# Performance work log

Hardware: AMD Instinct MI355X
Metric: run time of the kernel (lower is better)

## Reference

```python
import jax, jax.numpy as jnp
import numpy as np

LMAX = 6
BLOCK_SIZES = [(2 * l + 1) ** 2 for l in range(LMAX + 1)]  # [1,9,25,49,81,121,169], sum=455
IRREPS_DIM = sum(BLOCK_SIZES)


def setup_inputs() -> dict:
    key = jax.random.key(0)
    k1, k2, k3 = jax.random.split(key, 3)
    B, F_IN, F_OUT, N_GRID = 256, 128, 128, 512
    x = jax.random.normal(k1, (B, F_IN, IRREPS_DIM), dtype=jnp.float32)
    w = jax.random.normal(k2, (F_IN, F_OUT, N_GRID), dtype=jnp.float32)
    D = jax.random.normal(k3, (N_GRID, IRREPS_DIM), dtype=jnp.float32)
    return {"x": x, "w": w, "D": D}


def _so3_linear(x, psi):
    # x: [B, f_in, 455], psi: [f_in, f_out, 455]
    # Per-degree grouped linear: for each l, input block is (mul=2l+1, dim=2l+1),
    # weight block is (mul_in=2l+1, mul_out=2l+1); e3nn normalization 1/sqrt(f_in*mul_in).
    B, f_in, _ = x.shape
    f_out = psi.shape[1]
    outs = []
    off = 0
    for l in range(LMAX + 1):
        d = 2 * l + 1
        sz = d * d
        xb = x[:, :, off:off + sz].reshape(B, f_in, d, d)          # [B,f,u,i]
        wb = psi[:, :, off:off + sz].reshape(f_in, f_out, d, d)    # [f,g,u,v]
        yb = jnp.einsum('bfui,fguv->bgvi', xb, wb) / np.sqrt(f_in * d).astype(np.float32)
        outs.append(yb.reshape(B, f_out, sz))
        off += sz
    return jnp.concatenate(outs, axis=-1)  # [B, f_out, 455]


def reference(x, w, D):
    n_grid = D.shape[0]
    # Kernel synthesis from Wigner-D buffer: psi[f,g,i] = sum_n D[n,i] * w[f,g,n] / sqrt(n_grid)
    psi = jnp.einsum('ni,xyn->xyi', D, w) / np.float32(np.sqrt(n_grid))
    return _so3_linear(x, psi)
```

## Files before the change

kernel.cpp:

```cpp
#include <hip/hip_runtime.h>
#include <math.h>


typedef float f32x4 __attribute__((ext_vector_type(4)));
typedef short short8 __attribute__((ext_vector_type(8)));
typedef short short4v __attribute__((ext_vector_type(4)));
typedef __bf16 bf8 __attribute__((ext_vector_type(8)));

static __device__ inline bf8 as_bf8(short8 s) {
    union { short8 s; bf8 b; } u; u.s = s; return u.b;
}
static __device__ inline short f2bf(float f) {
    union { float f; unsigned u; } v; v.f = f;
    unsigned r = v.u + 0x7FFFu + ((v.u >> 16) & 1u);
    return (short)(r >> 16);
}
static __device__ __forceinline__ void glds16(const short* g, short* l) {
    __builtin_amdgcn_global_load_lds(
        (const __attribute__((address_space(1))) unsigned*)g,
        (__attribute__((address_space(3))) unsigned*)l, 16, 0, 0);
}

static const int OFFS_H[8] = {0, 1, 10, 35, 84, 165, 286, 455};
static const size_t PSIOFF_H[7] = {0, 16384, 163840, 573440, 1376256, 2703360, 4685824};
static const size_t XPOFF_H[7] = {0, 32768, 327680, 1146880, 2752512, 5406720, 9371648};
__constant__ int OFFS_D[8] = {0, 1, 10, 35, 84, 165, 286, 455};
__constant__ unsigned PSIOFF_D[7] = {0, 16384, 163840, 573440, 1376256, 2703360, 4685824};
__constant__ unsigned XPOFF_D[7] = {0, 32768, 327680, 1146880, 2752512, 5406720, 9371648};
__constant__ int PSTART_D[7] = {0, 676, 1160, 1484, 1680, 1780, 1816};

__global__ void transpose_D(const float* __restrict__ D, short* __restrict__ DT) {
    int idx = blockIdx.x * 256 + threadIdx.x;
    if (idx >= 455 * 512) return;
    int n = idx & 511, c = idx >> 9;
    DT[(size_t)c * 512 + n] = f2bf(D[(size_t)n * 455 + c]);
}

__global__ __launch_bounds__(256) void pack_x_all(const float* __restrict__ x,
                                                  short* __restrict__ XPall) {
    const int id = blockIdx.x;
    const int l = 6 - (id >> 10);
    const int local = id & 1023;
    const int fc = local & 3, b = local >> 2;
    const int d = 2 * l + 1, sz = d * d, off = OFFS_D[l];
    const int K = 128 * d;

    __shared__ short Ls[32][170];
    const int tid = threadIdx.x;
    const float* xb = x + ((size_t)b * 128 + fc * 32) * 455 + off;
    const int total = 32 * sz;
    for (int e = tid; e < total; e += 256) {
        int ff = e / sz, t = e - ff * sz;
        Ls[ff][t] = f2bf(xb[(size_t)ff * 455 + t]);
    }
    __syncthreads();
    short* XP = XPall + XPOFF_D[l];
    const int row = 32 * d;
    for (int e = tid; e < total; e += 256) {
        int i = e / row;
        int rem = e - i * row;
        int ff = rem / d, u = rem - ff * d;
        XP[((size_t)b * d + i) * K + (fc * 32 + ff) * d + u] = Ls[ff][u * d + i];
    }
}

template <int d>
__global__ __launch_bounds__(256) void pack_x(const float* __restrict__ x,
                                              short* __restrict__ XP, int off) {
    constexpr int sz = d * d;
    constexpr int K = 128 * d;
    const int fc = blockIdx.x, b = blockIdx.y;
    __shared__ short Ls[64][sz + 1];
    const int tid = threadIdx.x;
    const float* xb = x + ((size_t)b * 128 + fc * 64) * 455 + off;
    for (int e = tid; e < 64 * sz; e += 256) {
        int ff = e / sz, t = e - ff * sz;
        Ls[ff][t] = f2bf(xb[(size_t)ff * 455 + t]);
    }
    __syncthreads();
    for (int e = tid; e < 64 * sz; e += 256) {
        int i = e / (64 * d);
        int rem = e - i * (64 * d);
        int ff = rem / d, u = rem - ff * d;
        XP[((size_t)b * d + i) * K + (fc * 64 + ff) * d + u] = Ls[ff][u * d + i];
    }
}

template <int d>
__global__ __launch_bounds__(256) void psi_gemm(const float* __restrict__ w,
                                                const short* __restrict__ DT,
                                                short* __restrict__ PSI, int off) {
    constexpr int sz = d * d;
    constexpr int KP = 128 * d;
    const int mt = blockIdx.x;
    const int nt = blockIdx.y;
    const int tid = threadIdx.x, wave = tid >> 6, lane = tid & 63;
    const int wm = (wave & 1) * 32, wn = (wave >> 1) * 64;

    __shared__ short As[64][72];
    __shared__ short Bs[128][72];

    const float* Ag = w + (size_t)(mt * 64) * 512;
    f32x4 acc[2][4] = {};

    for (int k0 = 0; k0 < 512; k0 += 64) {
        __syncthreads();
#pragma unroll
        for (int c = 0; c < 4; ++c) {
            int e = (tid + c * 256) * 4;
            int r = e >> 6, cc = e & 63;
            float4 v = *reinterpret_cast<const float4*>(Ag + (size_t)r * 512 + k0 + cc);
            short4v s;
            s.x = f2bf(v.x); s.y = f2bf(v.y); s.z = f2bf(v.z); s.w = f2bf(v.w);
            *reinterpret_cast<short4v*>(&As[r][cc]) = s;
        }
#pragma unroll
        for (int c = 0; c < 4; ++c) {
            int ch = tid + c * 256;
            int r = ch >> 3, cc = (ch & 7) * 8;
            int gc = nt * 128 + r;
            int row = off + (gc < sz ? gc : 0);
            short8 v = *reinterpret_cast<const short8*>(DT + (size_t)row * 512 + k0 + cc);
            *reinterpret_cast<short8*>(&Bs[r][cc]) = v;
        }
        __syncthreads();
#pragma unroll
        for (int kf = 0; kf < 2; ++kf) {
            const int kc = kf * 32 + (lane >> 4) * 8;
            short8 af[2], bfr[4];
#pragma unroll
            for (int mi = 0; mi < 2; ++mi)
                af[mi] = *reinterpret_cast<const short8*>(&As[wm + mi * 16 + (lane & 15)][kc]);
#pragma unroll
            for (int ni = 0; ni < 4; ++ni)
                bfr[ni] = *reinterpret_cast<const short8*>(&Bs[wn + ni * 16 + (lane & 15)][kc]);
#pragma unroll
            for (int mi = 0; mi < 2; ++mi)
#pragma unroll
                for (int ni = 0; ni < 4; ++ni)
                    acc[mi][ni] = __builtin_amdgcn_mfma_f32_16x16x32_bf16(
                        as_bf8(af[mi]), as_bf8(bfr[ni]), acc[mi][ni], 0, 0, 0);
        }
    }

    const float s1 = 0.044194173824159216f;
#pragma unroll
    for (int mi = 0; mi < 2; ++mi)
#pragma unroll
        for (int ni = 0; ni < 4; ++ni) {
            int cix = nt * 128 + wn + ni * 16 + (lane & 15);
            if (cix < sz) {
                int u = cix / d, v = cix - u * d;
#pragma unroll
                for (int r = 0; r < 4; ++r) {
                    int m = mt * 64 + wm + mi * 16 + (lane >> 4) * 4 + r;
                    int f = m >> 7, g = m & 127;
                    PSI[(size_t)(g * d + v) * KP + f * d + u] = f2bf(acc[mi][ni][r] * s1);
                }
            }
        }
}

__global__ __launch_bounds__(256) void psi_gemm_all(const float* __restrict__ w,
                                                    const short* __restrict__ DT,
                                                    short* __restrict__ PSIall) {
    int id = blockIdx.y * gridDim.x + blockIdx.x;
    id = (id & 7) * 128 + (id >> 3);
    const int nt = id & 3, mt = id >> 2;
    const int tid = threadIdx.x, wave = tid >> 6, lane = tid & 63;
    const int wm = (wave & 1) * 32, wn = (wave >> 1) * 64;

    __shared__ short As[64][72];
    __shared__ short Bs[128][72];
    __shared__ int colInfo[128];

    if (tid < 128) {
        int cp = nt * 128 + tid;
        int info = -1;
        if (cp < 455) {
            int l = 6;
            while (OFFS_D[l] > cp) --l;
            int t = cp - OFFS_D[l];
            int d = 2 * l + 1;
            int v = t / d, u = t - v * d;
            info = (OFFS_D[l] + u * d + v) | (u << 9) | (v << 13) | (l << 17);
        }
        colInfo[tid] = info;
    }
    __syncthreads();

    int brow[4];
#pragma unroll
    for (int c = 0; c < 4; ++c) {
        int inf = colInfo[(tid + c * 256) >> 3];
        brow[c] = (inf < 0) ? 0 : (inf & 511);
    }

    const float* Ag = w + (size_t)(mt * 64) * 512;
    f32x4 acc[2][4] = {};

    for (int k0 = 0; k0 < 512; k0 += 64) {
        __syncthreads();
#pragma unroll
        for (int c = 0; c < 4; ++c) {
            int e = (tid + c * 256) * 4;
            int r = e >> 6, cc = e & 63;
            float4 v = *reinterpret_cast<const float4*>(Ag + (size_t)r * 512 + k0 + cc);
            short4v s;
            s.x = f2bf(v.x); s.y = f2bf(v.y); s.z = f2bf(v.z); s.w = f2bf(v.w);
            *reinterpret_cast<short4v*>(&As[r][cc]) = s;
        }
#pragma unroll
        for (int c = 0; c < 4; ++c) {
            int ch = tid + c * 256;
            int r = ch >> 3, cc = (ch & 7) * 8;
            short8 v = *reinterpret_cast<const short8*>(DT + (size_t)brow[c] * 512 + k0 + cc);
            *reinterpret_cast<short8*>(&Bs[r][cc]) = v;
        }
        __syncthreads();
#pragma unroll
        for (int kf = 0; kf < 2; ++kf) {
            const int kc = kf * 32 + (lane >> 4) * 8;
            short8 af[2], bfr[4];
#pragma unroll
            for (int mi = 0; mi < 2; ++mi)
                af[mi] = *reinterpret_cast<const short8*>(&As[wm + mi * 16 + (lane & 15)][kc]);
#pragma unroll
            for (int ni = 0; ni < 4; ++ni)
                bfr[ni] = *reinterpret_cast<const short8*>(&Bs[wn + ni * 16 + (lane & 15)][kc]);
#pragma unroll
            for (int mi = 0; mi < 2; ++mi)
#pragma unroll
                for (int ni = 0; ni < 4; ++ni)
                    acc[mi][ni] = __builtin_amdgcn_mfma_f32_16x16x32_bf16(
                        as_bf8(af[mi]), as_bf8(bfr[ni]), acc[mi][ni], 0, 0, 0);
        }
    }

    const float s1 = 0.044194173824159216f;
    const int f = mt >> 1;
#pragma unroll
    for (int mi = 0; mi < 2; ++mi)
#pragma unroll
        for (int ni = 0; ni < 4; ++ni) {
            int inf = colInfo[wn + ni * 16 + (lane & 15)];
            if (inf >= 0) {
                int u = (inf >> 9) & 15, v = (inf >> 13) & 15, l = (inf >> 17) & 7;
                int d = 2 * l + 1;
                size_t base = PSIOFF_D[l];
#pragma unroll
                for (int r = 0; r < 4; ++r) {
                    int m = mt * 64 + wm + mi * 16 + (lane >> 4) * 4 + r;
                    int g = m & 127;
                    PSIall[base + (size_t)(g * d + v) * (128 * d) + f * d + u] =
                        f2bf(acc[mi][ni][r] * s1);
                }
            }
        }
}

__global__ __launch_bounds__(256) void so3_gemm_all(const short* __restrict__ XPall,
                                                    const short* __restrict__ PSIall,
                                                    float* __restrict__ out) {
    const int p = blockIdx.x;
    int j = 6;
    while (PSTART_D[j] > p) --j;
    const int l = 6 - j;
    const int d = 2 * l + 1;
    const int pp = p - PSTART_D[j];
    const int S = 4 * d * d;
    {
    }
    const int q = S >> 3, rr = 4;
    const int xcd = pp & 7, pos = pp >> 3;
    const int local = (xcd < rr ? xcd * (q + 1) : rr * (q + 1) + (xcd - rr) * q) + pos;
    const int mtiles = 2 * d;
    const int mt = local % mtiles, nt = local / mtiles;
    const int K = 128 * d;
    const int off = OFFS_D[l];

    const int tid = threadIdx.x, wave = tid >> 6, lane = tid & 63;
    const int wm = (wave & 1) * 32, wn = (wave >> 1) * 64;

    __shared__ short As[64 * 64];
    __shared__ short Bs[128 * 64];

    const short* Ag = PSIall + PSIOFF_D[l] + (size_t)(mt * 64) * K;
    const short* Bg = XPall + XPOFF_D[l] + (size_t)(nt * 128) * K;

    const int lrow = lane >> 3;
    const int scol = (((lane & 7) ^ lrow) << 3);
    f32x4 acc[2][4] = {};

    for (int k0 = 0; k0 < K; k0 += 64) {
        __syncthreads();
#pragma unroll
        for (int c = 0; c < 2; ++c)
            glds16(Ag + (size_t)(wave * 16 + 8 * c + lrow) * K + k0 + scol,
                   &As[(wave * 16 + 8 * c) * 64]);
#pragma unroll
        for (int c = 0; c < 4; ++c)
            glds16(Bg + (size_t)(wave * 32 + 8 * c + lrow) * K + k0 + scol,
                   &Bs[(wave * 32 + 8 * c) * 64]);
        __syncthreads();
#pragma unroll
        for (int kf = 0; kf < 2; ++kf) {
            const int so = (((kf * 4 + (lane >> 4)) ^ (lane & 7)) << 3);
            short8 af[2], bfr[4];
#pragma unroll
            for (int mi = 0; mi < 2; ++mi)
                af[mi] = *reinterpret_cast<const short8*>(
                    &As[(wm + mi * 16 + (lane & 15)) * 64 + so]);
#pragma unroll
            for (int ni = 0; ni < 4; ++ni)
                bfr[ni] = *reinterpret_cast<const short8*>(
                    &Bs[(wn + ni * 16 + (lane & 15)) * 64 + so]);
#pragma unroll
            for (int mi = 0; mi < 2; ++mi)
#pragma unroll
                for (int ni = 0; ni < 4; ++ni)
                    acc[mi][ni] = __builtin_amdgcn_mfma_f32_16x16x32_bf16(
                        as_bf8(af[mi]), as_bf8(bfr[ni]), acc[mi][ni], 0, 0, 0);
        }
    }

    const float s2 = rsqrtf(128.0f * (float)d);
#pragma unroll
    for (int mi = 0; mi < 2; ++mi)
#pragma unroll
        for (int ni = 0; ni < 4; ++ni) {
            int n = nt * 128 + wn + ni * 16 + (lane & 15);
            int b = n / d, i = n - b * d;
#pragma unroll
            for (int r = 0; r < 4; ++r) {
                int m = mt * 64 + wm + mi * 16 + (lane >> 4) * 4 + r;
                int g = m / d, v = m - g * d;
                out[((size_t)b * 128 + g) * 455 + off + v * d + i] = acc[mi][ni][r] * s2;
            }
        }
}

template <int d>
__global__ __launch_bounds__(256) void so3_gemm_fb(const short* __restrict__ XP,
                                                   const short* __restrict__ PSI,
                                                   float* __restrict__ out, int off) {
    constexpr int K = 128 * d;
    constexpr int GX = 2 * d;
    constexpr int NWG = 4 * d * d;
    int id = blockIdx.y * gridDim.x + blockIdx.x;
    {
        constexpr int q = NWG >> 3, rr = NWG & 7;
        int xcd = id & 7, pos = id >> 3;
        id = (xcd < rr ? xcd * (q + 1) : rr * (q + 1) + (xcd - rr) * q) + pos;
    }
    const int mt = id % GX, nt = id / GX;
    const int tid = threadIdx.x, wave = tid >> 6, lane = tid & 63;
    const int wm = (wave & 1) * 32, wn = (wave >> 1) * 64;

    __shared__ short As[64][72];
    __shared__ short Bs[128][72];

    const short* Ag = PSI + (size_t)(mt * 64) * K;
    const short* Bg = XP + (size_t)(nt * 128) * K;
    f32x4 acc[2][4] = {};

    for (int k0 = 0; k0 < K; k0 += 64) {
        __syncthreads();
#pragma unroll
        for (int c = 0; c < 2; ++c) {
            int ch = tid + c * 256;
            int r = ch >> 3, cc = (ch & 7) * 8;
            *reinterpret_cast<short8*>(&As[r][cc]) =
                *reinterpret_cast<const short8*>(Ag + (size_t)r * K + k0 + cc);
        }
#pragma unroll
        for (int c = 0; c < 4; ++c) {
            int ch = tid + c * 256;
            int r = ch >> 3, cc = (ch & 7) * 8;
            *reinterpret_cast<short8*>(&Bs[r][cc]) =
                *reinterpret_cast<const short8*>(Bg + (size_t)r * K + k0 + cc);
        }
        __syncthreads();
#pragma unroll
        for (int kf = 0; kf < 2; ++kf) {
            const int kc = kf * 32 + (lane >> 4) * 8;
            short8 af[2], bfr[4];
#pragma unroll
            for (int mi = 0; mi < 2; ++mi)
                af[mi] = *reinterpret_cast<const short8*>(&As[wm + mi * 16 + (lane & 15)][kc]);
#pragma unroll
            for (int ni = 0; ni < 4; ++ni)
                bfr[ni] = *reinterpret_cast<const short8*>(&Bs[wn + ni * 16 + (lane & 15)][kc]);
#pragma unroll
            for (int mi = 0; mi < 2; ++mi)
#pragma unroll
                for (int ni = 0; ni < 4; ++ni)
                    acc[mi][ni] = __builtin_amdgcn_mfma_f32_16x16x32_bf16(
                        as_bf8(af[mi]), as_bf8(bfr[ni]), acc[mi][ni], 0, 0, 0);
        }
    }

    const float s2 = rsqrtf(128.0f * (float)d);
#pragma unroll
    for (int mi = 0; mi < 2; ++mi)
#pragma unroll
        for (int ni = 0; ni < 4; ++ni) {
            int n = nt * 128 + wn + ni * 16 + (lane & 15);
            int b = n / d, i = n - b * d;
#pragma unroll
            for (int r = 0; r < 4; ++r) {
                int m = mt * 64 + wm + mi * 16 + (lane >> 4) * 4 + r;
                int g = m / d, v = m - g * d;
                out[((size_t)b * 128 + g) * 455 + off + v * d + i] = acc[mi][ni][r] * s2;
            }
        }
}

template <int l>
static void run_l_fb(const float* x, const float* w, const short* DT, short* PSIbase,
                     short* XP, float* out, bool fused, hipStream_t stream) {
    constexpr int d = 2 * l + 1;
    const int off = OFFS_H[l];
    if (!fused) {
        constexpr int sz = d * d;
        constexpr int ntiles = (sz + 127) / 128;
        psi_gemm<d><<<dim3(256, ntiles), 256, 0, stream>>>(w, DT, PSIbase, off);
    }
    pack_x<d><<<dim3(2, 256), 256, 0, stream>>>(x, XP, off);
    const short* P = fused ? (PSIbase + PSIOFF_H[l]) : PSIbase;
    so3_gemm_fb<d><<<dim3(2 * d, 2 * d), 256, 0, stream>>>(XP, P, out, off);
}

extern "C" void kernel_launch(void* const* d_in, const int* in_sizes, int n_in,
                              void* d_out, int out_size, void* d_ws, size_t ws_size,
                              hipStream_t stream) {
    const float* x = (const float*)d_in[0];
    const float* w = (const float*)d_in[1];
    const float* D = (const float*)d_in[2];
    float* out = (float*)d_out;

    char* ws = (char*)d_ws;
    const size_t dtBytes      = (size_t)455 * 512 * 2;
    const size_t psiAllBytes  = (size_t)7454720 * 2;
    const size_t psiSlotBytes = (size_t)1664 * 1664 * 2;
    const size_t xpL6Bytes    = (size_t)3328 * 1664 * 2;
    const size_t xpAllBytes   = (size_t)14909440 * 2;

    short* DT = (short*)ws;
    transpose_D<<<(455 * 512 + 255) / 256, 256, 0, stream>>>(D, DT);

    if (ws_size >= dtBytes + psiAllBytes + xpAllBytes) {
        short* PSIall = (short*)(ws + dtBytes);
        short* XPall  = (short*)(ws + dtBytes + psiAllBytes);
        psi_gemm_all<<<dim3(4, 256), 256, 0, stream>>>(w, DT, PSIall);
        pack_x_all<<<dim3(7168), 256, 0, stream>>>(x, XPall);
        so3_gemm_all<<<dim3(1820), 256, 0, stream>>>(XPall, PSIall, out);
        return;
    }

    const bool fused = ws_size >= dtBytes + psiAllBytes + xpL6Bytes;
    short* PSIbase = (short*)(ws + dtBytes);
    short* XP = (short*)(ws + dtBytes + (fused ? psiAllBytes : psiSlotBytes));
    if (fused)
        psi_gemm_all<<<dim3(4, 256), 256, 0, stream>>>(w, DT, PSIbase);

    run_l_fb<0>(x, w, DT, PSIbase, XP, out, fused, stream);
    run_l_fb<1>(x, w, DT, PSIbase, XP, out, fused, stream);
    run_l_fb<2>(x, w, DT, PSIbase, XP, out, fused, stream);
    run_l_fb<3>(x, w, DT, PSIbase, XP, out, fused, stream);
    run_l_fb<4>(x, w, DT, PSIbase, XP, out, fused, stream);
    run_l_fb<5>(x, w, DT, PSIbase, XP, out, fused, stream);
    run_l_fb<6>(x, w, DT, PSIbase, XP, out, fused, stream);
}
```

Before: 138.8 us.

## Merge psi GEMM and x packing into one launch; enlarge so3 GEMM tiles

Merges the psi synthesis GEMM and the x packing kernel into a single prep_all launch that dispatches on block index, so the two independent stages share one grid and skip a kernel launch and the gap between them. The main so3 GEMM tile grows from 64x128 to 128x128 per workgroup, with each wave holding a 4x4 grid of MFMA accumulators. This halves the workgroup count and the redundant loads of the X operand. The cost is more registers and LDS per block and fewer blocks for occupancy, plus coarser load balance across the l-degree groups.

```diff
diff --git a/kernel.cpp b/kernel.cpp
--- a/kernel.cpp
+++ b/kernel.cpp
@@ -27,7 +27,7 @@
 __constant__ int OFFS_D[8] = {0, 1, 10, 35, 84, 165, 286, 455};
 __constant__ unsigned PSIOFF_D[7] = {0, 16384, 163840, 573440, 1376256, 2703360, 4685824};
 __constant__ unsigned XPOFF_D[7] = {0, 32768, 327680, 1146880, 2752512, 5406720, 9371648};
-__constant__ int PSTART_D[7] = {0, 676, 1160, 1484, 1680, 1780, 1816};
+__constant__ int PSTART2_D[7] = {0, 338, 580, 742, 840, 890, 908};
 
 __global__ void transpose_D(const float* __restrict__ D, short* __restrict__ DT) {
     int idx = blockIdx.x * 256 + threadIdx.x;
@@ -36,16 +36,110 @@
     DT[(size_t)c * 512 + n] = f2bf(D[(size_t)n * 455 + c]);
 }
 
-__global__ __launch_bounds__(256) void pack_x_all(const float* __restrict__ x,
-                                                  short* __restrict__ XPall) {
-    const int id = blockIdx.x;
+static __device__ __forceinline__ void psi_body(int rawid, const float* __restrict__ w,
+                                                const short* __restrict__ DT,
+                                                short* __restrict__ PSIall,
+                                                short (*As)[72], short (*Bs)[72],
+                                                int* colInfo) {
+    int id = (rawid & 7) * 128 + (rawid >> 3);
+    const int nt = id & 3, mt = id >> 2;
+    const int tid = threadIdx.x, wave = tid >> 6, lane = tid & 63;
+    const int wm = (wave & 1) * 32, wn = (wave >> 1) * 64;
+
+    if (tid < 128) {
+        int cp = nt * 128 + tid;
+        int info = -1;
+        if (cp < 455) {
+            int l = 6;
+            while (OFFS_D[l] > cp) --l;
+            int t = cp - OFFS_D[l];
+            int d = 2 * l + 1;
+            int v = t / d, u = t - v * d;
+            info = (OFFS_D[l] + u * d + v) | (u << 9) | (v << 13) | (l << 17);
+        }
+        colInfo[tid] = info;
+    }
+    __syncthreads();
+
+    int brow[4];
+#pragma unroll
+    for (int c = 0; c < 4; ++c) {
+        int inf = colInfo[(tid + c * 256) >> 3];
+        brow[c] = (inf < 0) ? 0 : (inf & 511);
+    }
+
+    const float* Ag = w + (size_t)(mt * 64) * 512;
+    f32x4 acc[2][4] = {};
+
+    for (int k0 = 0; k0 < 512; k0 += 64) {
+        __syncthreads();
+#pragma unroll
+        for (int c = 0; c < 4; ++c) {
+            int e = (tid + c * 256) * 4;
+            int r = e >> 6, cc = e & 63;
+            float4 v = *reinterpret_cast<const float4*>(Ag + (size_t)r * 512 + k0 + cc);
+            short4v s;
+            s.x = f2bf(v.x); s.y = f2bf(v.y); s.z = f2bf(v.z); s.w = f2bf(v.w);
+            *reinterpret_cast<short4v*>(&As[r][cc]) = s;
+        }
+#pragma unroll
+        for (int c = 0; c < 4; ++c) {
+            int ch = tid + c * 256;
+            int r = ch >> 3, cc = (ch & 7) * 8;
+            short8 v = *reinterpret_cast<const short8*>(DT + (size_t)brow[c] * 512 + k0 + cc);
+            *reinterpret_cast<short8*>(&Bs[r][cc]) = v;
+        }
+        __syncthreads();
+#pragma unroll
+        for (int kf = 0; kf < 2; ++kf) {
+            const int kc = kf * 32 + (lane >> 4) * 8;
+            short8 af[2], bfr[4];
+#pragma unroll
+            for (int mi = 0; mi < 2; ++mi)
+                af[mi] = *reinterpret_cast<const short8*>(&As[wm + mi * 16 + (lane & 15)][kc]);
+#pragma unroll
+            for (int ni = 0; ni < 4; ++ni)
+                bfr[ni] = *reinterpret_cast<const short8*>(&Bs[wn + ni * 16 + (lane & 15)][kc]);
+#pragma unroll
+            for (int mi = 0; mi < 2; ++mi)
+#pragma unroll
+                for (int ni = 0; ni < 4; ++ni)
+                    acc[mi][ni] = __builtin_amdgcn_mfma_f32_16x16x32_bf16(
+                        as_bf8(af[mi]), as_bf8(bfr[ni]), acc[mi][ni], 0, 0, 0);
+        }
+    }
+
+    const float s1 = 0.044194173824159216f;
+    const int f = mt >> 1;
+#pragma unroll
+    for (int mi = 0; mi < 2; ++mi)
+#pragma unroll
+        for (int ni = 0; ni < 4; ++ni) {
+            int inf = colInfo[wn + ni * 16 + (lane & 15)];
+            if (inf >= 0) {
+                int u = (inf >> 9) & 15, v = (inf >> 13) & 15, l = (inf >> 17) & 7;
+                int d = 2 * l + 1;
+                size_t base = PSIOFF_D[l];
+#pragma unroll
+                for (int r = 0; r < 4; ++r) {
+                    int m = mt * 64 + wm + mi * 16 + (lane >> 4) * 4 + r;
+                    int g = m & 127;
+                    PSIall[base + (size_t)(g * d + v) * (128 * d) + f * d + u] =
+                        f2bf(acc[mi][ni][r] * s1);
+                }
+            }
+        }
+}
+
+static __device__ __forceinline__ void pack_body(int id, const float* __restrict__ x,
+                                                 short* __restrict__ XPall,
+                                                 short (*Ls)[170]) {
     const int l = 6 - (id >> 10);
     const int local = id & 1023;
     const int fc = local & 3, b = local >> 2;
     const int d = 2 * l + 1, sz = d * d, off = OFFS_D[l];
     const int K = 128 * d;
 
-    __shared__ short Ls[32][170];
     const int tid = threadIdx.x;
     const float* xb = x + ((size_t)b * 128 + fc * 32) * 455 + off;
     const int total = 32 * sz;
@@ -62,6 +156,33 @@
         int ff = rem / d, u = rem - ff * d;
         XP[((size_t)b * d + i) * K + (fc * 32 + ff) * d + u] = Ls[ff][u * d + i];
     }
+}
+
+__global__ __launch_bounds__(256) void prep_all(const float* __restrict__ w,
+                                                const short* __restrict__ DT,
+                                                const float* __restrict__ x,
+                                                short* __restrict__ PSIall,
+                                                short* __restrict__ XPall) {
+    __shared__ __align__(16) char smem[28160];
+    const int bid = blockIdx.x;
+    if (bid < 1024) {
+        short (*As)[72] = (short(*)[72])smem;
+        short (*Bs)[72] = (short(*)[72])(smem + 9216);
+        int* colInfo = (int*)(smem + 27648);
+        psi_body(bid, w, DT, PSIall, As, Bs, colInfo);
+    } else {
+        short (*Ls)[170] = (short(*)[170])smem;
+        pack_body(bid - 1024, x, XPall, Ls);
+    }
+}
+
+__global__ __launch_bounds__(256) void psi_gemm_all(const float* __restrict__ w,
+                                                    const short* __restrict__ DT,
+                                                    short* __restrict__ PSIall) {
+    __shared__ short As[64][72];
+    __shared__ short Bs[128][72];
+    __shared__ int colInfo[128];
+    psi_body(blockIdx.y * gridDim.x + blockIdx.x, w, DT, PSIall, As, Bs, colInfo);
 }
 
 template <int d>
@@ -161,154 +282,53 @@
         }
 }
 
-__global__ __launch_bounds__(256) void psi_gemm_all(const float* __restrict__ w,
-                                                    const short* __restrict__ DT,
-                                                    short* __restrict__ PSIall) {
-    int id = blockIdx.y * gridDim.x + blockIdx.x;
-    id = (id & 7) * 128 + (id >> 3);
-    const int nt = id & 3, mt = id >> 2;
-    const int tid = threadIdx.x, wave = tid >> 6, lane = tid & 63;
-    const int wm = (wave & 1) * 32, wn = (wave >> 1) * 64;
-
-    __shared__ short As[64][72];
-    __shared__ short Bs[128][72];
-    __shared__ int colInfo[128];
-
-    if (tid < 128) {
-        int cp = nt * 128 + tid;
-        int info = -1;
-        if (cp < 455) {
-            int l = 6;
-            while (OFFS_D[l] > cp) --l;
-            int t = cp - OFFS_D[l];
-            int d = 2 * l + 1;
-            int v = t / d, u = t - v * d;
-            info = (OFFS_D[l] + u * d + v) | (u << 9) | (v << 13) | (l << 17);
-        }
-        colInfo[tid] = info;
-    }
-    __syncthreads();
-
-    int brow[4];
-#pragma unroll
-    for (int c = 0; c < 4; ++c) {
-        int inf = colInfo[(tid + c * 256) >> 3];
-        brow[c] = (inf < 0) ? 0 : (inf & 511);
-    }
-
-    const float* Ag = w + (size_t)(mt * 64) * 512;
-    f32x4 acc[2][4] = {};
-
-    for (int k0 = 0; k0 < 512; k0 += 64) {
-        __syncthreads();
-#pragma unroll
-        for (int c = 0; c < 4; ++c) {
-            int e = (tid + c * 256) * 4;
-            int r = e >> 6, cc = e & 63;
-            float4 v = *reinterpret_cast<const float4*>(Ag + (size_t)r * 512 + k0 + cc);
-            short4v s;
-            s.x = f2bf(v.x); s.y = f2bf(v.y); s.z = f2bf(v.z); s.w = f2bf(v.w);
-            *reinterpret_cast<short4v*>(&As[r][cc]) = s;
-        }
-#pragma unroll
-        for (int c = 0; c < 4; ++c) {
-            int ch = tid + c * 256;
-            int r = ch >> 3, cc = (ch & 7) * 8;
-            short8 v = *reinterpret_cast<const short8*>(DT + (size_t)brow[c] * 512 + k0 + cc);
-            *reinterpret_cast<short8*>(&Bs[r][cc]) = v;
-        }
-        __syncthreads();
-#pragma unroll
-        for (int kf = 0; kf < 2; ++kf) {
-            const int kc = kf * 32 + (lane >> 4) * 8;
-            short8 af[2], bfr[4];
-#pragma unroll
-            for (int mi = 0; mi < 2; ++mi)
-                af[mi] = *reinterpret_cast<const short8*>(&As[wm + mi * 16 + (lane & 15)][kc]);
-#pragma unroll
-            for (int ni = 0; ni < 4; ++ni)
-                bfr[ni] = *reinterpret_cast<const short8*>(&Bs[wn + ni * 16 + (lane & 15)][kc]);
-#pragma unroll
-            for (int mi = 0; mi < 2; ++mi)
-#pragma unroll
-                for (int ni = 0; ni < 4; ++ni)
-                    acc[mi][ni] = __builtin_amdgcn_mfma_f32_16x16x32_bf16(
-                        as_bf8(af[mi]), as_bf8(bfr[ni]), acc[mi][ni], 0, 0, 0);
-        }
-    }
-
-    const float s1 = 0.044194173824159216f;
-    const int f = mt >> 1;
-#pragma unroll
-    for (int mi = 0; mi < 2; ++mi)
-#pragma unroll
-        for (int ni = 0; ni < 4; ++ni) {
-            int inf = colInfo[wn + ni * 16 + (lane & 15)];
-            if (inf >= 0) {
-                int u = (inf >> 9) & 15, v = (inf >> 13) & 15, l = (inf >> 17) & 7;
-                int d = 2 * l + 1;
-                size_t base = PSIOFF_D[l];
-#pragma unroll
-                for (int r = 0; r < 4; ++r) {
-                    int m = mt * 64 + wm + mi * 16 + (lane >> 4) * 4 + r;
-                    int g = m & 127;
-                    PSIall[base + (size_t)(g * d + v) * (128 * d) + f * d + u] =
-                        f2bf(acc[mi][ni][r] * s1);
-                }
-            }
-        }
-}
-
 __global__ __launch_bounds__(256) void so3_gemm_all(const short* __restrict__ XPall,
                                                     const short* __restrict__ PSIall,
                                                     float* __restrict__ out) {
     const int p = blockIdx.x;
     int j = 6;
-    while (PSTART_D[j] > p) --j;
+    while (PSTART2_D[j] > p) --j;
     const int l = 6 - j;
     const int d = 2 * l + 1;
-    const int pp = p - PSTART_D[j];
-    const int S = 4 * d * d;
-    {
-    }
-    const int q = S >> 3, rr = 4;
+    const int pp = p - PSTART2_D[j];
+    const int S = 2 * d * d;
+    const int q = S >> 3;
     const int xcd = pp & 7, pos = pp >> 3;
-    const int local = (xcd < rr ? xcd * (q + 1) : rr * (q + 1) + (xcd - rr) * q) + pos;
-    const int mtiles = 2 * d;
-    const int mt = local % mtiles, nt = local / mtiles;
+    const int local = (xcd < 2 ? xcd * (q + 1) : 2 * (q + 1) + (xcd - 2) * q) + pos;
+    const int mt = local % d, nt = local / d;
     const int K = 128 * d;
     const int off = OFFS_D[l];
 
     const int tid = threadIdx.x, wave = tid >> 6, lane = tid & 63;
-    const int wm = (wave & 1) * 32, wn = (wave >> 1) * 64;
-
-    __shared__ short As[64 * 64];
+    const int wm = (wave & 1) * 64, wn = (wave >> 1) * 64;
+
+    __shared__ short As[128 * 64];
     __shared__ short Bs[128 * 64];
 
-    const short* Ag = PSIall + PSIOFF_D[l] + (size_t)(mt * 64) * K;
+    const short* Ag = PSIall + PSIOFF_D[l] + (size_t)(mt * 128) * K;
     const short* Bg = XPall + XPOFF_D[l] + (size_t)(nt * 128) * K;
 
-    const int lrow = lane >> 3;
-    const int scol = (((lane & 7) ^ lrow) << 3);
-    f32x4 acc[2][4] = {};
+    const int srow = wave * 32 + (lane >> 3);
+    const int scol = (((lane & 7) ^ (lane >> 3)) << 3);
+    f32x4 acc[4][4] = {};
 
     for (int k0 = 0; k0 < K; k0 += 64) {
         __syncthreads();
 #pragma unroll
-        for (int c = 0; c < 2; ++c)
-            glds16(Ag + (size_t)(wave * 16 + 8 * c + lrow) * K + k0 + scol,
-                   &As[(wave * 16 + 8 * c) * 64]);
-#pragma unroll
         for (int c = 0; c < 4; ++c)
-            glds16(Bg + (size_t)(wave * 32 + 8 * c + lrow) * K + k0 + scol,
+            glds16(Ag + (size_t)(srow + 8 * c) * K + k0 + scol,
+                   &As[(wave * 32 + 8 * c) * 64]);
+#pragma unroll
+        for (int c = 0; c < 4; ++c)
+            glds16(Bg + (size_t)(srow + 8 * c) * K + k0 + scol,
                    &Bs[(wave * 32 + 8 * c) * 64]);
         __syncthreads();
 #pragma unroll
         for (int kf = 0; kf < 2; ++kf) {
             const int so = (((kf * 4 + (lane >> 4)) ^ (lane & 7)) << 3);
-            short8 af[2], bfr[4];
-#pragma unroll
-            for (int mi = 0; mi < 2; ++mi)
+            short8 af[4], bfr[4];
+#pragma unroll
+            for (int mi = 0; mi < 4; ++mi)
                 af[mi] = *reinterpret_cast<const short8*>(
                     &As[(wm + mi * 16 + (lane & 15)) * 64 + so]);
 #pragma unroll
@@ -316,7 +336,7 @@
                 bfr[ni] = *reinterpret_cast<const short8*>(
                     &Bs[(wn + ni * 16 + (lane & 15)) * 64 + so]);
 #pragma unroll
-            for (int mi = 0; mi < 2; ++mi)
+            for (int mi = 0; mi < 4; ++mi)
 #pragma unroll
                 for (int ni = 0; ni < 4; ++ni)
                     acc[mi][ni] = __builtin_amdgcn_mfma_f32_16x16x32_bf16(
@@ -326,14 +346,14 @@
 
     const float s2 = rsqrtf(128.0f * (float)d);
 #pragma unroll
-    for (int mi = 0; mi < 2; ++mi)
+    for (int mi = 0; mi < 4; ++mi)
 #pragma unroll
         for (int ni = 0; ni < 4; ++ni) {
             int n = nt * 128 + wn + ni * 16 + (lane & 15);
             int b = n / d, i = n - b * d;
 #pragma unroll
             for (int r = 0; r < 4; ++r) {
-                int m = mt * 64 + wm + mi * 16 + (lane >> 4) * 4 + r;
+                int m = mt * 128 + wm + mi * 16 + (lane >> 4) * 4 + r;
                 int g = m / d, v = m - g * d;
                 out[((size_t)b * 128 + g) * 455 + off + v * d + i] = acc[mi][ni][r] * s2;
             }
@@ -452,9 +472,8 @@
     if (ws_size >= dtBytes + psiAllBytes + xpAllBytes) {
         short* PSIall = (short*)(ws + dtBytes);
         short* XPall  = (short*)(ws + dtBytes + psiAllBytes);
-        psi_gemm_all<<<dim3(4, 256), 256, 0, stream>>>(w, DT, PSIall);
-        pack_x_all<<<dim3(7168), 256, 0, stream>>>(x, XPall);
-        so3_gemm_all<<<dim3(1820), 256, 0, stream>>>(XPall, PSIall, out);
+        prep_all<<<dim3(8192), 256, 0, stream>>>(w, DT, x, PSIall, XPall);
+        so3_gemm_all<<<dim3(910), 256, 0, stream>>>(XPall, PSIall, out);
         return;
     }
 
```

New measurement: 136.2 us. About the same (-1.8%).

## Merge psi GEMM and x packing into one launch; templatize so3 GEMM per degree

Applied to the files above, without the earlier changes.

The psi synthesis GEMM and the x packing kernel become a single prep_all launch, with blocks 0-1023 doing psi tiles and the rest packing x. Each pack block now loads all 455 columns for 32 features once and writes every degree's slice, instead of running one block per degree. The so3 GEMM dispatches to a templated body per degree so d, K, offsets and tile counts are compile-time constants, and the k loop is left un-unrolled. The goal is to cut a kernel launch, repeated x reads and runtime integer division, at the cost of larger shared memory per block and mixed work within one grid.

```diff
diff --git a/kernel.cpp b/kernel.cpp
--- a/kernel.cpp
+++ b/kernel.cpp
@@ -23,11 +23,10 @@
 
 static const int OFFS_H[8] = {0, 1, 10, 35, 84, 165, 286, 455};
 static const size_t PSIOFF_H[7] = {0, 16384, 163840, 573440, 1376256, 2703360, 4685824};
-static const size_t XPOFF_H[7] = {0, 32768, 327680, 1146880, 2752512, 5406720, 9371648};
+static constexpr unsigned PSIOFF_C[7] = {0, 16384, 163840, 573440, 1376256, 2703360, 4685824};
+static constexpr unsigned XPOFF_C[7] = {0, 32768, 327680, 1146880, 2752512, 5406720, 9371648};
 __constant__ int OFFS_D[8] = {0, 1, 10, 35, 84, 165, 286, 455};
 __constant__ unsigned PSIOFF_D[7] = {0, 16384, 163840, 573440, 1376256, 2703360, 4685824};
-__constant__ unsigned XPOFF_D[7] = {0, 32768, 327680, 1146880, 2752512, 5406720, 9371648};
-__constant__ int PSTART_D[7] = {0, 676, 1160, 1484, 1680, 1780, 1816};
 
 __global__ void transpose_D(const float* __restrict__ D, short* __restrict__ DT) {
     int idx = blockIdx.x * 256 + threadIdx.x;
@@ -36,32 +35,160 @@
     DT[(size_t)c * 512 + n] = f2bf(D[(size_t)n * 455 + c]);
 }
 
-__global__ __launch_bounds__(256) void pack_x_all(const float* __restrict__ x,
+static __device__ __forceinline__ void psi_body(int rawid, const float* __restrict__ w,
+                                                const short* __restrict__ DT,
+                                                short* __restrict__ PSIall,
+                                                short (*As)[72], short (*Bs)[72],
+                                                int* colInfo) {
+    int id = (rawid & 7) * 128 + (rawid >> 3);
+    const int nt = id & 3, mt = id >> 2;
+    const int tid = threadIdx.x, wave = tid >> 6, lane = tid & 63;
+    const int wm = (wave & 1) * 32, wn = (wave >> 1) * 64;
+
+    if (tid < 128) {
+        int cp = nt * 128 + tid;
+        int info = -1;
+        if (cp < 455) {
+            int l = 6;
+            while (OFFS_D[l] > cp) --l;
+            int t = cp - OFFS_D[l];
+            int d = 2 * l + 1;
+            int v = t / d, u = t - v * d;
+            info = (OFFS_D[l] + u * d + v) | (u << 9) | (v << 13) | (l << 17);
+        }
+        colInfo[tid] = info;
+    }
+    __syncthreads();
+
+    int brow[4];
+#pragma unroll
+    for (int c = 0; c < 4; ++c) {
+        int inf = colInfo[(tid + c * 256) >> 3];
+        brow[c] = (inf < 0) ? 0 : (inf & 511);
+    }
+
+    const float* Ag = w + (size_t)(mt * 64) * 512;
+    f32x4 acc[2][4] = {};
+
+    for (int k0 = 0; k0 < 512; k0 += 64) {
+        __syncthreads();
+#pragma unroll
+        for (int c = 0; c < 4; ++c) {
+            int e = (tid + c * 256) * 4;
+            int r = e >> 6, cc = e & 63;
+            float4 v = *reinterpret_cast<const float4*>(Ag + (size_t)r * 512 + k0 + cc);
+            short4v s;
+            s.x = f2bf(v.x); s.y = f2bf(v.y); s.z = f2bf(v.z); s.w = f2bf(v.w);
+            *reinterpret_cast<short4v*>(&As[r][cc]) = s;
+        }
+#pragma unroll
+        for (int c = 0; c < 4; ++c) {
+            int ch = tid + c * 256;
+            int r = ch >> 3, cc = (ch & 7) * 8;
+            short8 v = *reinterpret_cast<const short8*>(DT + (size_t)brow[c] * 512 + k0 + cc);
+            *reinterpret_cast<short8*>(&Bs[r][cc]) = v;
+        }
+        __syncthreads();
+#pragma unroll
+        for (int kf = 0; kf < 2; ++kf) {
+            const int kc = kf * 32 + (lane >> 4) * 8;
+            short8 af[2], bfr[4];
+#pragma unroll
+            for (int mi = 0; mi < 2; ++mi)
+                af[mi] = *reinterpret_cast<const short8*>(&As[wm + mi * 16 + (lane & 15)][kc]);
+#pragma unroll
+            for (int ni = 0; ni < 4; ++ni)
+                bfr[ni] = *reinterpret_cast<const short8*>(&Bs[wn + ni * 16 + (lane & 15)][kc]);
+#pragma unroll
+            for (int mi = 0; mi < 2; ++mi)
+#pragma unroll
+                for (int ni = 0; ni < 4; ++ni)
+                    acc[mi][ni] = __builtin_amdgcn_mfma_f32_16x16x32_bf16(
+                        as_bf8(af[mi]), as_bf8(bfr[ni]), acc[mi][ni], 0, 0, 0);
+        }
+    }
+
+    const float s1 = 0.044194173824159216f;
+    const int f = mt >> 1;
+#pragma unroll
+    for (int mi = 0; mi < 2; ++mi)
+#pragma unroll
+        for (int ni = 0; ni < 4; ++ni) {
+            int inf = colInfo[wn + ni * 16 + (lane & 15)];
+            if (inf >= 0) {
+                int u = (inf >> 9) & 15, v = (inf >> 13) & 15, l = (inf >> 17) & 7;
+                int d = 2 * l + 1;
+                size_t base = PSIOFF_D[l];
+#pragma unroll
+                for (int r = 0; r < 4; ++r) {
+                    int m = mt * 64 + wm + mi * 16 + (lane >> 4) * 4 + r;
+                    int g = m & 127;
+                    PSIall[base + (size_t)(g * d + v) * (128 * d) + f * d + u] =
+                        f2bf(acc[mi][ni][r] * s1);
+                }
+            }
+        }
+}
+
+template <int l>
+static __device__ __forceinline__ void pack_slice(int b, int fc,
+                                                  const short (*Ls)[458],
                                                   short* __restrict__ XPall) {
-    const int id = blockIdx.x;
-    const int l = 6 - (id >> 10);
-    const int local = id & 1023;
-    const int fc = local & 3, b = local >> 2;
-    const int d = 2 * l + 1, sz = d * d, off = OFFS_D[l];
-    const int K = 128 * d;
-
-    __shared__ short Ls[32][170];
-    const int tid = threadIdx.x;
-    const float* xb = x + ((size_t)b * 128 + fc * 32) * 455 + off;
-    const int total = 32 * sz;
-    for (int e = tid; e < total; e += 256) {
-        int ff = e / sz, t = e - ff * sz;
-        Ls[ff][t] = f2bf(xb[(size_t)ff * 455 + t]);
-    }
-    __syncthreads();
-    short* XP = XPall + XPOFF_D[l];
-    const int row = 32 * d;
-    for (int e = tid; e < total; e += 256) {
+    constexpr int d = 2 * l + 1;
+    constexpr int sz = d * d;
+    constexpr int K = 128 * d;
+    constexpr int off = l * (2 * l - 1) * (2 * l + 1) / 3;
+    constexpr int row = 32 * d;
+    constexpr int total = 32 * sz;
+    short* XP = XPall + XPOFF_C[l];
+    for (int e = threadIdx.x; e < total; e += 256) {
         int i = e / row;
         int rem = e - i * row;
         int ff = rem / d, u = rem - ff * d;
-        XP[((size_t)b * d + i) * K + (fc * 32 + ff) * d + u] = Ls[ff][u * d + i];
-    }
+        XP[((size_t)b * d + i) * K + (fc * 32 + ff) * d + u] = Ls[ff][off + u * d + i];
+    }
+}
+
+__global__ __launch_bounds__(256) void prep_all(const float* __restrict__ w,
+                                                const short* __restrict__ DT,
+                                                const float* __restrict__ x,
+                                                short* __restrict__ PSIall,
+                                                short* __restrict__ XPall) {
+    __shared__ __align__(16) char smem[29312];
+    const int bid = blockIdx.x;
+    if (bid < 1024) {
+        short (*As)[72] = (short(*)[72])smem;
+        short (*Bs)[72] = (short(*)[72])(smem + 9216);
+        int* colInfo = (int*)(smem + 27648);
+        psi_body(bid, w, DT, PSIall, As, Bs, colInfo);
+    } else {
+        const int local = bid - 1024;
+        const int fc = local & 3, b = local >> 2;
+        short (*Ls)[458] = (short(*)[458])smem;
+        const float* xb = x + ((size_t)b * 128 + fc * 32) * 455;
+        const int tid = threadIdx.x;
+        for (int e = tid; e < 32 * 455; e += 256) {
+            int ff = e / 455, t = e - ff * 455;
+            Ls[ff][t] = f2bf(xb[(size_t)ff * 455 + t]);
+        }
+        __syncthreads();
+        pack_slice<6>(b, fc, Ls, XPall);
+        pack_slice<5>(b, fc, Ls, XPall);
+        pack_slice<4>(b, fc, Ls, XPall);
+        pack_slice<3>(b, fc, Ls, XPall);
+        pack_slice<2>(b, fc, Ls, XPall);
+        pack_slice<1>(b, fc, Ls, XPall);
+        pack_slice<0>(b, fc, Ls, XPall);
+    }
+}
+
+__global__ __launch_bounds__(256) void psi_gemm_all(const float* __restrict__ w,
+                                                    const short* __restrict__ DT,
+                                                    short* __restrict__ PSIall) {
+    __shared__ short As[64][72];
+    __shared__ short Bs[128][72];
+    __shared__ int colInfo[128];
+    psi_body(blockIdx.y * gridDim.x + blockIdx.x, w, DT, PSIall, As, Bs, colInfo);
 }
 
 template <int d>
@@ -161,137 +288,35 @@
         }
 }
 
-__global__ __launch_bounds__(256) void psi_gemm_all(const float* __restrict__ w,
-                                                    const short* __restrict__ DT,
-                                                    short* __restrict__ PSIall) {
-    int id = blockIdx.y * gridDim.x + blockIdx.x;
-    id = (id & 7) * 128 + (id >> 3);
-    const int nt = id & 3, mt = id >> 2;
+template <int l>
+static __device__ __forceinline__ void so3_body(int pp,
+                                                const short* __restrict__ XPall,
+                                                const short* __restrict__ PSIall,
+                                                float* __restrict__ out,
+                                                short* As, short* Bs) {
+    constexpr int d = 2 * l + 1;
+    constexpr int K = 128 * d;
+    constexpr int S = 4 * d * d;
+    constexpr int q = S >> 3;
+    constexpr int off = l * (2 * l - 1) * (2 * l + 1) / 3;
+    constexpr int mtiles = 2 * d;
+
+    const int xcd = pp & 7, pos = pp >> 3;
+    const int local = (xcd < 4 ? xcd * (q + 1) : 4 * (q + 1) + (xcd - 4) * q) + pos;
+    const int mt = local % mtiles, nt = local / mtiles;
+
     const int tid = threadIdx.x, wave = tid >> 6, lane = tid & 63;
     const int wm = (wave & 1) * 32, wn = (wave >> 1) * 64;
 
-    __shared__ short As[64][72];
-    __shared__ short Bs[128][72];
-    __shared__ int colInfo[128];
-
-    if (tid < 128) {
-        int cp = nt * 128 + tid;
-        int info = -1;
-        if (cp < 455) {
-            int l = 6;
-            while (OFFS_D[l] > cp) --l;
-            int t = cp - OFFS_D[l];
-            int d = 2 * l + 1;
-            int v = t / d, u = t - v * d;
-            info = (OFFS_D[l] + u * d + v) | (u << 9) | (v << 13) | (l << 17);
-        }
-        colInfo[tid] = info;
-    }
-    __syncthreads();
-
-    int brow[4];
-#pragma unroll
-    for (int c = 0; c < 4; ++c) {
-        int inf = colInfo[(tid + c * 256) >> 3];
-        brow[c] = (inf < 0) ? 0 : (inf & 511);
-    }
-
-    const float* Ag = w + (size_t)(mt * 64) * 512;
-    f32x4 acc[2][4] = {};
-
-    for (int k0 = 0; k0 < 512; k0 += 64) {
-        __syncthreads();
-#pragma unroll
-        for (int c = 0; c < 4; ++c) {
-            int e = (tid + c * 256) * 4;
-            int r = e >> 6, cc = e & 63;
-            float4 v = *reinterpret_cast<const float4*>(Ag + (size_t)r * 512 + k0 + cc);
-            short4v s;
-            s.x = f2bf(v.x); s.y = f2bf(v.y); s.z = f2bf(v.z); s.w = f2bf(v.w);
-            *reinterpret_cast<short4v*>(&As[r][cc]) = s;
-        }
-#pragma unroll
-        for (int c = 0; c < 4; ++c) {
-            int ch = tid + c * 256;
-            int r = ch >> 3, cc = (ch & 7) * 8;
-            short8 v = *reinterpret_cast<const short8*>(DT + (size_t)brow[c] * 512 + k0 + cc);
-            *reinterpret_cast<short8*>(&Bs[r][cc]) = v;
-        }
-        __syncthreads();
-#pragma unroll
-        for (int kf = 0; kf < 2; ++kf) {
-            const int kc = kf * 32 + (lane >> 4) * 8;
-            short8 af[2], bfr[4];
-#pragma unroll
-            for (int mi = 0; mi < 2; ++mi)
-                af[mi] = *reinterpret_cast<const short8*>(&As[wm + mi * 16 + (lane & 15)][kc]);
-#pragma unroll
-            for (int ni = 0; ni < 4; ++ni)
-                bfr[ni] = *reinterpret_cast<const short8*>(&Bs[wn + ni * 16 + (lane & 15)][kc]);
-#pragma unroll
-            for (int mi = 0; mi < 2; ++mi)
-#pragma unroll
-                for (int ni = 0; ni < 4; ++ni)
-                    acc[mi][ni] = __builtin_amdgcn_mfma_f32_16x16x32_bf16(
-                        as_bf8(af[mi]), as_bf8(bfr[ni]), acc[mi][ni], 0, 0, 0);
-        }
-    }
-
-    const float s1 = 0.044194173824159216f;
-    const int f = mt >> 1;
-#pragma unroll
-    for (int mi = 0; mi < 2; ++mi)
-#pragma unroll
-        for (int ni = 0; ni < 4; ++ni) {
-            int inf = colInfo[wn + ni * 16 + (lane & 15)];
-            if (inf >= 0) {
-                int u = (inf >> 9) & 15, v = (inf >> 13) & 15, l = (inf >> 17) & 7;
-                int d = 2 * l + 1;
-                size_t base = PSIOFF_D[l];
-#pragma unroll
-                for (int r = 0; r < 4; ++r) {
-                    int m = mt * 64 + wm + mi * 16 + (lane >> 4) * 4 + r;
-                    int g = m & 127;
-                    PSIall[base + (size_t)(g * d + v) * (128 * d) + f * d + u] =
-                        f2bf(acc[mi][ni][r] * s1);
-                }
-            }
-        }
-}
-
-__global__ __launch_bounds__(256) void so3_gemm_all(const short* __restrict__ XPall,
-                                                    const short* __restrict__ PSIall,
-                                                    float* __restrict__ out) {
-    const int p = blockIdx.x;
-    int j = 6;
-    while (PSTART_D[j] > p) --j;
-    const int l = 6 - j;
-    const int d = 2 * l + 1;
-    const int pp = p - PSTART_D[j];
-    const int S = 4 * d * d;
-    {
-    }
-    const int q = S >> 3, rr = 4;
-    const int xcd = pp & 7, pos = pp >> 3;
-    const int local = (xcd < rr ? xcd * (q + 1) : rr * (q + 1) + (xcd - rr) * q) + pos;
-    const int mtiles = 2 * d;
-    const int mt = local % mtiles, nt = local / mtiles;
-    const int K = 128 * d;
-    const int off = OFFS_D[l];
-
-    const int tid = threadIdx.x, wave = tid >> 6, lane = tid & 63;
-    const int wm = (wave & 1) * 32, wn = (wave >> 1) * 64;
-
-    __shared__ short As[64 * 64];
-    __shared__ short Bs[128 * 64];
-
-    const short* Ag = PSIall + PSIOFF_D[l] + (size_t)(mt * 64) * K;
-    const short* Bg = XPall + XPOFF_D[l] + (size_t)(nt * 128) * K;
+    const short* Ag = PSIall + PSIOFF_C[l] + (size_t)(mt * 64) * K;
+    const short* Bg = XPall + XPOFF_C[l] + (size_t)(nt * 128) * K;
 
     const int lrow = lane >> 3;
     const int scol = (((lane & 7) ^ lrow) << 3);
+
     f32x4 acc[2][4] = {};
 
+#pragma unroll 1
     for (int k0 = 0; k0 < K; k0 += 64) {
         __syncthreads();
 #pragma unroll
@@ -338,6 +363,21 @@
                 out[((size_t)b * 128 + g) * 455 + off + v * d + i] = acc[mi][ni][r] * s2;
             }
         }
+}
+
+__global__ __launch_bounds__(256) void so3_gemm_all(const short* __restrict__ XPall,
+                                                    const short* __restrict__ PSIall,
+                                                    float* __restrict__ out) {
+    __shared__ short As[64 * 64];
+    __shared__ short Bs[128 * 64];
+    const int p = blockIdx.x;
+    if (p < 676)       so3_body<6>(p,        XPall, PSIall, out, As, Bs);
+    else if (p < 1160) so3_body<5>(p - 676,  XPall, PSIall, out, As, Bs);
+    else if (p < 1484) so3_body<4>(p - 1160, XPall, PSIall, out, As, Bs);
+    else if (p < 1680) so3_body<3>(p - 1484, XPall, PSIall, out, As, Bs);
+    else if (p < 1780) so3_body<2>(p - 1680, XPall, PSIall, out, As, Bs);
+    else if (p < 1816) so3_body<1>(p - 1780, XPall, PSIall, out, As, Bs);
+    else               so3_body<0>(p - 1816, XPall, PSIall, out, As, Bs);
 }
 
 template <int d>
@@ -452,8 +492,7 @@
     if (ws_size >= dtBytes + psiAllBytes + xpAllBytes) {
         short* PSIall = (short*)(ws + dtBytes);
         short* XPall  = (short*)(ws + dtBytes + psiAllBytes);
-        psi_gemm_all<<<dim3(4, 256), 256, 0, stream>>>(w, DT, PSIall);
-        pack_x_all<<<dim3(7168), 256, 0, stream>>>(x, XPall);
+        prep_all<<<dim3(2048), 256, 0, stream>>>(w, DT, x, PSIall, XPall);
         so3_gemm_all<<<dim3(1820), 256, 0, stream>>>(XPall, PSIall, out);
         return;
     }
```

New measurement: 118.5 us. 1.17x faster.
